# Kernel optimization log

Measured on AMD Instinct MI355X. Metric: run time of the kernel, lower is better.

Reference implementation:

```python
import jax, jax.numpy as jnp
import numpy as np

B, L = 4, 2048
D_MODEL, D_INNER, D_STATE, DT_RANK, D_CONV = 1024, 2048, 16, 64, 4


def setup_inputs() -> dict:
    key = jax.random.key(0)
    ks = jax.random.split(key, 10)
    s = lambda k, shape, sc: jax.random.normal(k, shape, dtype=jnp.float32) * sc
    return {
        "x": s(ks[0], (B, L, D_MODEL), 1.0),
        "W_in": s(ks[1], (2 * D_INNER, D_MODEL), D_MODEL ** -0.5),
        "conv_w": s(ks[2], (D_INNER, D_CONV), D_CONV ** -0.5),
        "conv_b": s(ks[3], (D_INNER,), 0.02),
        "A_log": jnp.log(jnp.arange(1, D_STATE + 1, dtype=jnp.float32)),
        "D": jnp.ones((D_INNER,), dtype=jnp.float32),
        "W_x": s(ks[4], (DT_RANK + 2 * D_STATE, D_INNER), D_INNER ** -0.5),
        "W_dt": s(ks[5], (D_INNER, DT_RANK), DT_RANK ** -0.5),
        "b_dt": s(ks[6], (D_INNER,), 0.02) - 4.0,  # softplus -> small positive dt
        "W_out": s(ks[7], (D_MODEL, D_INNER), D_INNER ** -0.5),
    }


def reference(x, W_in, conv_w, conv_b, A_log, D, W_x, W_dt, b_dt, W_out):
    Bb, Ll, _ = x.shape
    # input projection, split into ssm branch and gate branch
    xz = x @ W_in.T                       # (B, L, 2*Di)
    xr, z = jnp.split(xz, 2, axis=-1)     # (B, L, Di) each
    # depthwise causal conv1d (torch pads both sides then slices [:L])
    xc = jax.lax.conv_general_dilated(
        xr.transpose(0, 2, 1),            # (B, Di, L)
        conv_w[:, None, :],               # (Di, 1, K)
        window_strides=(1,),
        padding=[(D_CONV - 1, 0)],
        dimension_numbers=("NCH", "OIH", "NCH"),
        feature_group_count=D_INNER,
    ) + conv_b[None, :, None]
    xs = jax.nn.silu(xc.transpose(0, 2, 1))  # (B, L, Di)
    # input-dependent dt, B, C
    x_dbl = xs @ W_x.T                        # (B, L, dt_rank + 2*S)
    dt_r, b_sel, c_sel = jnp.split(x_dbl, [DT_RANK, DT_RANK + D_STATE], axis=-1)
    dt = jax.nn.softplus(dt_r @ W_dt.T + b_dt)  # (B, L, Di)
    a_diag = -jnp.exp(A_log)                    # (S,)

    def step(h, inp):
        dt_t, b_t, c_t, x_t = inp                       # (B,Di),(B,S),(B,S),(B,Di)
        a_bar = jnp.exp(dt_t[:, :, None] * a_diag)      # (B, Di, S)
        h = a_bar * h + (dt_t * x_t)[:, :, None] * b_t[:, None, :]
        y = jnp.einsum("bds,bs->bd", h, c_t) + D * x_t
        return h, y

    h0 = jnp.zeros((Bb, D_INNER, D_STATE), dtype=x.dtype)
    _, ys = jax.lax.scan(
        step, h0,
        (dt.transpose(1, 0, 2), b_sel.transpose(1, 0, 2),
         c_sel.transpose(1, 0, 2), xs.transpose(1, 0, 2)),
    )
    y = ys.transpose(1, 0, 2)                           # (B, L, Di)
    return (y * jax.nn.silu(z)) @ W_out.T               # (B, L, d_model)
```

## Files before the change

kernel.cpp:

```cpp
#include <hip/hip_runtime.h>
#include <math.h>

typedef unsigned short u16;
typedef unsigned int u32;

constexpr int Bb = 4, Ll = 2048, DM = 1024, DI = 2048, DS = 16, DTR = 64, KC = 4;
constexpr int M = Bb * Ll;
constexpr int NPAD = 128;
constexpr int NCHUNK = 32;
constexpr int LC = Ll / NCHUNK;
constexpr int LDXZ = 4096;

__device__ __forceinline__ float b2f(u16 u) {
    return __uint_as_float(((u32)u) << 16);
}
__device__ __forceinline__ u16 f2b(float f) {
    u32 x = __float_as_uint(f);
    u32 r = (x + 0x7fffu + ((x >> 16) & 1u)) >> 16;
    return (u16)r;
}
__device__ __forceinline__ float softplus_fast(float v) {
    return (v > 20.f) ? v : __logf(1.f + __expf(v));
}

typedef __attribute__((ext_vector_type(8))) short short8;
typedef __attribute__((ext_vector_type(4))) short short4v;
typedef __attribute__((ext_vector_type(4))) float floatx4;

__device__ __forceinline__ void gload16(const u16* g, u16* l) {
    __builtin_amdgcn_global_load_lds(
        (const __attribute__((address_space(1))) void*)g,
        (__attribute__((address_space(3))) void*)l,
        16, 0, 0);
}

__device__ __forceinline__ void pow_tree(float a, float* aa) {
    float a2 = a * a, a4 = a2 * a2, a8 = a4 * a4;
    aa[0] = a;        aa[1] = a2;       aa[2] = a * a2;   aa[3] = a4;
    aa[4] = a * a4;   aa[5] = a2 * a4;  aa[6] = aa[2] * a4; aa[7] = a8;
    aa[8] = a * a8;   aa[9] = a2 * a8;  aa[10] = aa[2] * a8; aa[11] = a4 * a8;
    aa[12] = aa[4] * a8; aa[13] = aa[5] * a8; aa[14] = aa[6] * a8; aa[15] = a8 * a8;
}

template<int GX, int GY>
__device__ __forceinline__ void xcd_swizzle(int& bx, int& by) {
    const int bid = blockIdx.y * GX + blockIdx.x;
    const int xcd = bid & 7;
    const int i = bid >> 3;
    const int c_local = i >> 5;
    const int within = i & 31;
    const int lx = within & 7, ly = within >> 3;
    const int chunk = xcd + c_local * 8;
    constexpr int CXN = GX / 8;
    const int cx = chunk % CXN;
    const int cy = chunk / CXN;
    bx = cx * 8 + lx;
    by = cy * 4 + ly;
}

template<int OUTM>
__global__ __launch_bounds__(512, 2) void gemm256(
    const u16* __restrict__ A, const u16* __restrict__ Bm,
    void* __restrict__ Cv,
    int K, int lda, int ldb, int ldc)
{
    __shared__ alignas(16) u16 ldsA[4][256 * 32];
    __shared__ alignas(16) u16 ldsB[4][256 * 32];

    int bx, by;
    xcd_swizzle<16, 32>(bx, by);

    const int lane = threadIdx.x & 63;
    const int wave = threadIdx.x >> 6;
    const int wr = wave >> 2;
    const int wc = wave & 3;
    const int m0 = by * 256;
    const int n0 = bx * 256;

    const int lrow = lane >> 2;
    const int skc  = (((lane & 3) + (lane >> 3)) & 3) * 8;
    const u16* pA = A  + (size_t)(m0 + wave * 32 + lrow) * lda + skc;
    const u16* pB = Bm + (size_t)(n0 + wave * 32 + lrow) * ldb + skc;
    const int ldst = wave * 1024;

    const int r16 = lane & 15;
    const int quad = lane >> 4;
    const int slot = (quad + 4 - ((r16 >> 1) & 3)) & 3;
    const int aoff = (wr * 128 + r16) * 32 + slot * 8;
    const int boff = (wc * 64  + r16) * 32 + slot * 8;

    const int NT = K >> 5;

    floatx4 acc[8][4] = {};

#pragma unroll
    for (int t = 0; t < 3; ++t) {
        gload16(pA + t * 32,            &ldsA[t][ldst]);
        gload16(pA + t * 32 + 16 * lda, &ldsA[t][ldst + 512]);
        gload16(pB + t * 32,            &ldsB[t][ldst]);
        gload16(pB + t * 32 + 16 * ldb, &ldsB[t][ldst + 512]);
    }
    asm volatile("s_waitcnt vmcnt(8)" ::: "memory");
    __builtin_amdgcn_sched_barrier(0);
    __builtin_amdgcn_s_barrier();

    for (int t = 0; t < NT; ++t) {
        const u16* la = &ldsA[t & 3][aoff];
        const u16* lb = &ldsB[t & 3][boff];
        short8 af[8], bf[4];
#pragma unroll
        for (int i = 0; i < 8; ++i) af[i] = *(const short8*)(la + i * 512);
#pragma unroll
        for (int j = 0; j < 4; ++j) bf[j] = *(const short8*)(lb + j * 512);
        if (t + 3 < NT) {
            const u16* sA = pA + (t + 3) * 32;
            const u16* sB = pB + (t + 3) * 32;
            u16* dA = &ldsA[(t + 3) & 3][ldst];
            u16* dB = &ldsB[(t + 3) & 3][ldst];
            gload16(sA, dA);
            gload16(sA + 16 * lda, dA + 512);
            gload16(sB, dB);
            gload16(sB + 16 * ldb, dB + 512);
        }
        __builtin_amdgcn_sched_barrier(0);
        __builtin_amdgcn_s_barrier();
        asm volatile("s_waitcnt lgkmcnt(0)" ::: "memory");
        __builtin_amdgcn_sched_barrier(0);
        __builtin_amdgcn_s_setprio(1);
#pragma unroll
        for (int i = 0; i < 8; ++i)
#pragma unroll
            for (int j = 0; j < 4; ++j)
                acc[i][j] = __builtin_amdgcn_mfma_f32_16x16x32_bf16(
                    af[i], bf[j], acc[i][j], 0, 0, 0);
        __builtin_amdgcn_s_setprio(0);
        if (t + 3 < NT)      asm volatile("s_waitcnt vmcnt(8)" ::: "memory");
        else if (t + 2 < NT) asm volatile("s_waitcnt vmcnt(4)" ::: "memory");
        else if (t + 1 < NT) asm volatile("s_waitcnt vmcnt(0)" ::: "memory");
        __builtin_amdgcn_sched_barrier(0);
        __builtin_amdgcn_s_barrier();
    }

    const int mw = m0 + wr * 128;
    const int nw = n0 + wc * 64;
    const int rb = quad * 4;
#pragma unroll
    for (int i = 0; i < 8; ++i) {
#pragma unroll
        for (int j = 0; j < 4; ++j) {
            const int n = nw + j * 16 + r16;
#pragma unroll
            for (int r = 0; r < 4; ++r) {
                const int m = mw + i * 16 + rb + r;
                float v = acc[i][j][r];
                if (OUTM == 1)
                    ((float*)Cv)[(size_t)m * ldc + n] = v;
                else
                    ((u16*)Cv)[(size_t)m * ldc + n] = f2b(v);
            }
        }
    }
}

template<int OUTM>
__global__ __launch_bounds__(512, 4) void gemm256n128(
    const u16* __restrict__ A, const u16* __restrict__ Bm,
    void* __restrict__ Cv,
    int K, int lda, int ldb, int ldc)
{
    __shared__ alignas(16) u16 ldsA[3][256 * 32];
    __shared__ alignas(16) u16 ldsB[3][128 * 32];

    int bx, by;
    xcd_swizzle<8, 32>(bx, by);

    const int lane = threadIdx.x & 63;
    const int wave = threadIdx.x >> 6;
    const int wr = wave >> 1;
    const int wc = wave & 1;
    const int m0 = by * 256;
    const int n0 = bx * 128;

    const int lrow = lane >> 2;
    const int skc  = (((lane & 3) + (lane >> 3)) & 3) * 8;
    const u16* pA = A  + (size_t)(m0 + wave * 32 + lrow) * lda + skc;
    const u16* pB = Bm + (size_t)(n0 + wave * 16 + lrow) * ldb + skc;
    const int ldstA = wave * 1024;
    const int ldstB = wave * 512;

    const int r16 = lane & 15;
    const int quad = lane >> 4;
    const int slot = (quad + 4 - ((r16 >> 1) & 3)) & 3;
    const int aoff = (wr * 64 + r16) * 32 + slot * 8;
    const int boff = (wc * 64 + r16) * 32 + slot * 8;

    const int NT = K >> 5;

    floatx4 acc[4][4] = {};

#pragma unroll
    for (int t = 0; t < 2; ++t) {
        gload16(pA + t * 32,            &ldsA[t][ldstA]);
        gload16(pA + t * 32 + 16 * lda, &ldsA[t][ldstA + 512]);
        gload16(pB + t * 32,            &ldsB[t][ldstB]);
    }
    asm volatile("s_waitcnt vmcnt(3)" ::: "memory");
    __builtin_amdgcn_sched_barrier(0);
    __builtin_amdgcn_s_barrier();

    int bc = 0, bs = 2;
    for (int t = 0; t < NT; ++t) {
        const u16* la = &ldsA[bc][aoff];
        const u16* lb = &ldsB[bc][boff];
        short8 af[4], bf[4];
#pragma unroll
        for (int i = 0; i < 4; ++i) af[i] = *(const short8*)(la + i * 512);
#pragma unroll
        for (int j = 0; j < 4; ++j) bf[j] = *(const short8*)(lb + j * 512);
        if (t + 2 < NT) {
            const u16* sa = pA + (t + 2) * 32;
            u16* da = &ldsA[bs][ldstA];
            gload16(sa, da);
            gload16(sa + 16 * lda, da + 512);
            gload16(pB + (t + 2) * 32, &ldsB[bs][ldstB]);
        }
        __builtin_amdgcn_sched_barrier(0);
        __builtin_amdgcn_s_barrier();
        asm volatile("s_waitcnt lgkmcnt(0)" ::: "memory");
        __builtin_amdgcn_sched_barrier(0);
        __builtin_amdgcn_s_setprio(1);
#pragma unroll
        for (int i = 0; i < 4; ++i)
#pragma unroll
            for (int j = 0; j < 4; ++j)
                acc[i][j] = __builtin_amdgcn_mfma_f32_16x16x32_bf16(
                    af[i], bf[j], acc[i][j], 0, 0, 0);
        __builtin_amdgcn_s_setprio(0);
        if (t + 2 < NT)      asm volatile("s_waitcnt vmcnt(3)" ::: "memory");
        else if (t + 1 < NT) asm volatile("s_waitcnt vmcnt(0)" ::: "memory");
        __builtin_amdgcn_sched_barrier(0);
        __builtin_amdgcn_s_barrier();
        bc = (bc == 2) ? 0 : bc + 1;
        bs = (bs == 2) ? 0 : bs + 1;
    }

    const int mw = m0 + wr * 64;
    const int nw = n0 + wc * 64;
    const int rb = quad * 4;
#pragma unroll
    for (int i = 0; i < 4; ++i) {
#pragma unroll
        for (int j = 0; j < 4; ++j) {
            const int n = nw + j * 16 + r16;
#pragma unroll
            for (int r = 0; r < 4; ++r) {
                const int m = mw + i * 16 + rb + r;
                float v = acc[i][j][r];
                if (OUTM == 1)
                    ((float*)Cv)[(size_t)m * ldc + n] = v;
                else
                    ((u16*)Cv)[(size_t)m * ldc + n] = f2b(v);
            }
        }
    }
}

template<int OUTM>
__global__ __launch_bounds__(256) void gemm_bt(
    const u16* __restrict__ A, const u16* __restrict__ Bm,
    void* __restrict__ Cv, const float* __restrict__ bias,
    int K, int lda, int ldb, int ldc)
{
    __shared__ alignas(16) u16 ldsA[128 * 32];
    __shared__ alignas(16) u16 ldsB[128 * 32];

    const int lane = threadIdx.x & 63;
    const int wave = threadIdx.x >> 6;
    const int wr = wave >> 1, wc = wave & 1;
    const int m0 = blockIdx.y * 128;
    const int n0 = blockIdx.x * 128;
    const int koff = (OUTM == 4) ? blockIdx.z * K : 0;

    const int srow = wave * 32 + (lane >> 2);
    const int skc  = (((lane & 3) + (lane >> 3)) & 3) * 8;
    const u16* Ag = A + (size_t)(m0 + srow) * lda + skc + koff;
    const u16* Bg = Bm + (size_t)(n0 + srow) * ldb + skc + koff;
    u16* lA = &ldsA[wave * 1024];
    u16* lB = &ldsB[wave * 1024];

    const int r16 = lane & 15;
    const int quad = lane >> 4;
    const int slot = (quad + 4 - ((r16 >> 1) & 3)) & 3;
    const u16* arow = &ldsA[(wr * 64 + r16) * 32 + slot * 8];
    const u16* brow = &ldsB[(wc * 64 + r16) * 32 + slot * 8];

    floatx4 acc[4][4] = {};

    for (int k0 = 0; k0 < K; k0 += 32) {
        gload16(Ag + k0,                    lA);
        gload16(Ag + k0 + (size_t)16 * lda, lA + 512);
        gload16(Bg + k0,                    lB);
        gload16(Bg + k0 + (size_t)16 * ldb, lB + 512);
        __syncthreads();

        short8 af[4], bf[4];
#pragma unroll
        for (int i = 0; i < 4; i++) af[i] = *(const short8*)(arow + i * 16 * 32);
#pragma unroll
        for (int j = 0; j < 4; j++) bf[j] = *(const short8*)(brow + j * 16 * 32);
#pragma unroll
        for (int i = 0; i < 4; i++)
#pragma unroll
            for (int j = 0; j < 4; j++)
                acc[i][j] = __builtin_amdgcn_mfma_f32_16x16x32_bf16(
                    af[i], bf[j], acc[i][j], 0, 0, 0);
        __syncthreads();
    }

    const int mw = m0 + wr * 64;
    const int nw = n0 + wc * 64;
    const int rb = quad * 4;
#pragma unroll
    for (int i = 0; i < 4; i++) {
#pragma unroll
        for (int j = 0; j < 4; j++) {
            const int n = nw + j * 16 + r16;
            if (OUTM == 4 && n >= 96) continue;
#pragma unroll
            for (int r = 0; r < 4; r++) {
                const int m = mw + i * 16 + rb + r;
                float v = acc[i][j][r];
                if (OUTM == 2)
                    v = softplus_fast(v + bias[n]);
                if (OUTM == 4)
                    ((float*)Cv)[((size_t)blockIdx.z * M + m) * ldc + n] = v;
                else if (OUTM == 1)
                    ((float*)Cv)[(size_t)m * ldc + n] = v;
                else
                    ((u16*)Cv)[(size_t)m * ldc + n] = f2b(v);
            }
        }
    }
}

__global__ __launch_bounds__(256) void redk_gemm3(
    const float* __restrict__ part, u16* __restrict__ xdbl,
    float* __restrict__ bcf)
{
    const int t = blockIdx.x * 256 + threadIdx.x;
    const int c4 = t % 24;
    const int m = t / 24;
    const int n4 = c4 * 4;
    const size_t stride = (size_t)M * NPAD;
    const float* p = part + (size_t)m * NPAD + n4;
    floatx4 acc = *(const floatx4*)(p)
                + *(const floatx4*)(p + stride)
                + *(const floatx4*)(p + 2 * stride)
                + *(const floatx4*)(p + 3 * stride);
    if (n4 < 64) {
        short4v ob;
#pragma unroll
        for (int j = 0; j < 4; j++) ob[j] = (short)f2b(acc[j]);
        *(short4v*)(xdbl + (size_t)m * 64 + n4) = ob;
    } else {
        *(floatx4*)(bcf + (size_t)m * 32 + (n4 - 64)) = acc;
    }
}

__global__ __launch_bounds__(256) void prep_all(
    const float* __restrict__ x, const float* __restrict__ W_in,
    const float* __restrict__ W_x, const float* __restrict__ W_dt,
    const float* __restrict__ W_out,
    u16* __restrict__ xbf, u16* __restrict__ wibf, u16* __restrict__ wxp,
    u16* __restrict__ wdtb, u16* __restrict__ woutb)
{
    constexpr int N0 = M * DM;
    constexpr int N1 = 2 * DI * DM;
    constexpr int N2 = NPAD * DI;
    constexpr int N3 = DI * DTR;
    int idx = blockIdx.x * blockDim.x + threadIdx.x;
    if (idx < N0) {
        xbf[idx] = f2b(x[idx]);
        return;
    }
    idx -= N0;
    if (idx < N1) {
        wibf[idx] = f2b(W_in[idx]);
    } else if (idx < N1 + N2) {
        int i = idx - N1;
        int r = i >> 11, c = i & 2047;
        wxp[i] = (r < 96) ? f2b(W_x[r * 2048 + c]) : (u16)0;
    } else if (idx < N1 + N2 + N3) {
        int i = idx - N1 - N2;
        wdtb[i] = f2b(W_dt[i]);
    } else {
        int i = idx - N1 - N2 - N3;
        woutb[i] = f2b(W_out[i]);
    }
}

__global__ __launch_bounds__(256) void conv_silu(
    const u16* __restrict__ xz, const float* __restrict__ conv_w,
    const float* __restrict__ conv_b, u16* __restrict__ xs)
{
    const int m = blockIdx.x;
    const int d0 = threadIdx.x * 8;
    const int l = m & (Ll - 1);

    float acc[8];
    {
        floatx4 cb0 = *(const floatx4*)(conv_b + d0);
        floatx4 cb1 = *(const floatx4*)(conv_b + d0 + 4);
#pragma unroll
        for (int j = 0; j < 4; j++) { acc[j] = cb0[j]; acc[4 + j] = cb1[j]; }
    }
    float w[8][KC];
#pragma unroll
    for (int jd = 0; jd < 8; jd++) {
        floatx4 wv = *(const floatx4*)(conv_w + (d0 + jd) * KC);
#pragma unroll
        for (int k = 0; k < KC; k++) w[jd][k] = wv[k];
    }
#pragma unroll
    for (int k = 0; k < KC; k++) {
        int li = l - (KC - 1) + k;
        if (li >= 0) {
            short8 xv = *(const short8*)(xz + (size_t)(m - (KC - 1) + k) * LDXZ + d0);
#pragma unroll
            for (int jd = 0; jd < 8; jd++)
                acc[jd] += b2f((u16)xv[jd]) * w[jd][k];
        }
    }
    short8 o;
#pragma unroll
    for (int jd = 0; jd < 8; jd++) {
        float s = acc[jd] / (1.f + __expf(-acc[jd]));
        o[jd] = (short)f2b(s);
    }
    *(short8*)(xs + (size_t)m * DI + d0) = o;
}

__global__ __launch_bounds__(256) void scan_p1(
    const u16* __restrict__ xzdt, const u16* __restrict__ xs,
    const float* __restrict__ bcf, const float* __restrict__ A_log,
    float* __restrict__ scr_h, float* __restrict__ sdt_g)
{
    __shared__ alignas(16) float bcs[LC * 32];

    const int d = blockIdx.x * 256 + threadIdx.x;
    const int b = blockIdx.y;
    const int c = blockIdx.z;
    const int m0 = b * Ll + c * LC;

    {
        const float* bc_g = bcf + (size_t)m0 * 32;
#pragma unroll
        for (int j = 0; j < 2; j++) {
            int idx = j * 1024 + threadIdx.x * 4;
            *(floatx4*)(bcs + idx) = *(const floatx4*)(bc_g + idx);
        }
    }

    const float ad0 = -__expf(A_log[0]);
    float adl[DS];
    bool fast = true;
#pragma unroll
    for (int s = 0; s < DS; s++) {
        float av = -__expf(A_log[s]);
        adl[s] = av;
        float kr = (float)(s + 1);
        if (fabsf(av / ad0 - kr) > 1e-4f * kr) fast = false;
    }

    const u16* dt_p = xzdt + (size_t)m0 * LDXZ + d;
    const u16* xs_p = xs + (size_t)m0 * DI + d;

    float h[DS] = {};
    float sdt = 0.f;

    __syncthreads();

    u16 dt_c = dt_p[0],     xs_c = xs_p[0];
    u16 dt_1 = dt_p[LDXZ],  xs_1 = xs_p[DI];

    if (fast) {
        for (int l = 0; l < LC; l++) {
            u16 dt_2 = dt_p[2 * LDXZ];
            u16 xs_2 = xs_p[2 * DI];
            const float* bl = bcs + l * 32;
            floatx4 B0 = *(const floatx4*)(bl);
            floatx4 B1 = *(const floatx4*)(bl + 4);
            floatx4 B2 = *(const floatx4*)(bl + 8);
            floatx4 B3 = *(const floatx4*)(bl + 12);

            float dtv = b2f(dt_c);
            float xv  = b2f(xs_c);
            float bx = dtv * xv;
            sdt += dtv;
            float aa[DS];
            pow_tree(__expf(dtv * ad0), aa);
#pragma unroll
            for (int s = 0; s < DS; s++) {
                float Bv = (s < 4) ? B0[s] : (s < 8) ? B1[s - 4]
                         : (s < 12) ? B2[s - 8] : B3[s - 12];
                h[s] = aa[s] * h[s] + bx * Bv;
            }
            dt_c = dt_1; dt_1 = dt_2; xs_c = xs_1; xs_1 = xs_2;
            dt_p += LDXZ; xs_p += DI;
        }
    } else {
        for (int l = 0; l < LC; l++) {
            u16 dt_2 = dt_p[2 * LDXZ];
            u16 xs_2 = xs_p[2 * DI];
            const float* bl = bcs + l * 32;
            floatx4 B0 = *(const floatx4*)(bl);
            floatx4 B1 = *(const floatx4*)(bl + 4);
            floatx4 B2 = *(const floatx4*)(bl + 8);
            floatx4 B3 = *(const floatx4*)(bl + 12);

            float dtv = b2f(dt_c);
            float xv  = b2f(xs_c);
            float bx = dtv * xv;
            sdt += dtv;
#pragma unroll
            for (int s = 0; s < DS; s++) {
                float Bv = (s < 4) ? B0[s] : (s < 8) ? B1[s - 4]
                         : (s < 12) ? B2[s - 8] : B3[s - 12];
                float a = __expf(dtv * adl[s]);
                h[s] = a * h[s] + bx * Bv;
            }
            dt_c = dt_1; dt_1 = dt_2; xs_c = xs_1; xs_1 = xs_2;
            dt_p += LDXZ; xs_p += DI;
        }
    }

    const size_t base = ((size_t)(b * NCHUNK + c) * DI + d) * DS;
#pragma unroll
    for (int s = 0; s < DS; s += 4) {
        floatx4 hv = {h[s], h[s+1], h[s+2], h[s+3]};
        *(floatx4*)(scr_h + base + s) = hv;
    }
    sdt_g[(size_t)(b * NCHUNK + c) * DI + d] = sdt;
}

__global__ __launch_bounds__(256) void scan_p2(
    float* __restrict__ scr_h, const float* __restrict__ sdt_g,
    const float* __restrict__ A_log)
{
    const int t = blockIdx.x * 256 + threadIdx.x;
    const int s = t & 15;
    const int d = (t >> 4) & (DI - 1);
    const int b = t >> 15;
    const float adl = -__expf(A_log[s]);

    float hin = 0.f;
    for (int c0 = 0; c0 < NCHUNK; c0 += 8) {
        float he[8], P[8];
#pragma unroll
        for (int j = 0; j < 8; j++) {
            const size_t base = ((size_t)(b * NCHUNK + c0 + j) * DI + d) * DS + s;
            he[j] = scr_h[base];
            P[j] = adl * sdt_g[(size_t)(b * NCHUNK + c0 + j) * DI + d];
        }
#pragma unroll
        for (int j = 0; j < 8; j++) P[j] = __expf(P[j]);
#pragma unroll
        for (int j = 0; j < 8; j++) {
            const size_t base = ((size_t)(b * NCHUNK + c0 + j) * DI + d) * DS + s;
            scr_h[base] = hin;
            hin = P[j] * hin + he[j];
        }
    }
}

__global__ __launch_bounds__(256) void scan_p3(
    const u16* __restrict__ xz, const u16* xs, const float* __restrict__ bcf,
    const float* __restrict__ scr_hin, const float* __restrict__ A_log,
    const float* __restrict__ Dvec, u16* yg)
{
    __shared__ alignas(16) float bcs[LC * 32];

    const int d = blockIdx.x * 256 + threadIdx.x;
    const int b = blockIdx.y;
    const int c = blockIdx.z;
    const int m0 = b * Ll + c * LC;

    {
        const float* bc_g = bcf + (size_t)m0 * 32;
#pragma unroll
        for (int j = 0; j < 2; j++) {
            int idx = j * 1024 + threadIdx.x * 4;
            *(floatx4*)(bcs + idx) = *(const floatx4*)(bc_g + idx);
        }
    }

    const float ad0 = -__expf(A_log[0]);
    float adl[DS];
    bool fast = true;
#pragma unroll
    for (int s = 0; s < DS; s++) {
        float av = -__expf(A_log[s]);
        adl[s] = av;
        float kr = (float)(s + 1);
        if (fabsf(av / ad0 - kr) > 1e-4f * kr) fast = false;
    }
    const float Dd = Dvec[d];

    const u16* dt_p = xz + (size_t)m0 * LDXZ + d;
    const u16* z_p  = xz + (size_t)m0 * LDXZ + 2048 + d;
    const u16* xs_p = xs + (size_t)m0 * DI + d;
    u16* yg_p = yg + (size_t)m0 * DI + d;

    float h[DS];
    const size_t base = ((size_t)(b * NCHUNK + c) * DI + d) * DS;
#pragma unroll
    for (int s = 0; s < DS; s += 4) {
        floatx4 hv = *(const floatx4*)(scr_hin + base + s);
        h[s] = hv[0]; h[s+1] = hv[1]; h[s+2] = hv[2]; h[s+3] = hv[3];
    }

    __syncthreads();

    u16 dt_c = dt_p[0],    dt_1 = dt_p[LDXZ];
    u16 xs_c = xs_p[0],    xs_1 = xs_p[DI];
    u16 z_c  = z_p[0],     z_1  = z_p[LDXZ];

    for (int l = 0; l < LC; l++) {
        u16 dt_2 = dt_p[2 * LDXZ];
        u16 xs_2 = xs_p[2 * DI];
        u16 z_2  = z_p[2 * LDXZ];
        const float* bl = bcs + l * 32;
        floatx4 Bq[4], Cq[4];
#pragma unroll
        for (int q = 0; q < 4; q++) {
            Bq[q] = *(const floatx4*)(bl + q * 4);
            Cq[q] = *(const floatx4*)(bl + 16 + q * 4);
        }

        float dtv = b2f(dt_c);
        float xv  = b2f(xs_c);
        float bx = dtv * xv;
        float aa[DS];
        if (fast) {
            pow_tree(__expf(dtv * ad0), aa);
        } else {
#pragma unroll
            for (int s = 0; s < DS; s++) aa[s] = __expf(dtv * adl[s]);
        }
        float y0 = 0.f, y1 = 0.f, y2 = 0.f, y3 = 0.f;
#pragma unroll
        for (int q = 0; q < 4; q++) {
#pragma unroll
            for (int j = 0; j < 4; j++) {
                int s = q * 4 + j;
                h[s] = aa[s] * h[s] + bx * Bq[q][j];
            }
        }
#pragma unroll
        for (int j = 0; j < 4; j++) {
            y0 += h[j] * Cq[0][j];
            y1 += h[4 + j] * Cq[1][j];
            y2 += h[8 + j] * Cq[2][j];
            y3 += h[12 + j] * Cq[3][j];
        }
        float yt = ((y0 + y1) + (y2 + y3)) + Dd * xv;
        float zv = b2f(z_c);
        float g = zv / (1.f + __expf(-zv));
        yg_p[0] = f2b(yt * g);

        dt_c = dt_1; dt_1 = dt_2;
        xs_c = xs_1; xs_1 = xs_2;
        z_c  = z_1;  z_1  = z_2;
        dt_p += LDXZ; xs_p += DI; z_p += LDXZ; yg_p += DI;
    }
}

extern "C" void kernel_launch(void* const* d_in, const int* in_sizes, int n_in,
                              void* d_out, int out_size, void* d_ws, size_t ws_size,
                              hipStream_t stream)
{
    const float* x      = (const float*)d_in[0];
    const float* W_in   = (const float*)d_in[1];
    const float* conv_w = (const float*)d_in[2];
    const float* conv_b = (const float*)d_in[3];
    const float* A_log  = (const float*)d_in[4];
    const float* Dvec   = (const float*)d_in[5];
    const float* W_x    = (const float*)d_in[6];
    const float* W_dt   = (const float*)d_in[7];
    const float* b_dt   = (const float*)d_in[8];
    const float* W_out  = (const float*)d_in[9];

    u16* ws = (u16*)d_ws;
    u16* xz    = ws;                 ws += (size_t)M * LDXZ;
    u16* xs    = ws;                 ws += (size_t)M * DI;
    u16* xbf   = ws;                 ws += (size_t)M * DM;
    u16* wibf  = ws;                 ws += (size_t)2 * DI * DM;
    u16* wxp   = ws;                 ws += (size_t)NPAD * DI;
    u16* wdtb  = ws;                 ws += (size_t)DI * DTR;
    u16* woutb = ws;                 ws += (size_t)DM * DI;
    u16* xdbl  = ws;                 ws += (size_t)M * NPAD;
    float* part  = (float*)xbf;
    float* scr_h = (float*)xbf;
    float* bcf   = (float*)wibf;
    float* sdt_g = bcf + (size_t)M * 32;

    {
        constexpr int NTOT = M * DM + 2 * DI * DM + NPAD * DI + DI * DTR + DM * DI;
        prep_all<<<NTOT / 256, 256, 0, stream>>>(
            x, W_in, W_x, W_dt, W_out, xbf, wibf, wxp, wdtb, woutb);
    }

    gemm256<0><<<dim3(LDXZ / 256, M / 256), 512, 0, stream>>>(
        xbf, wibf, xz, DM, DM, DM, LDXZ);

    conv_silu<<<M, 256, 0, stream>>>(xz, conv_w, conv_b, xs);

    gemm_bt<4><<<dim3(1, M / 128, 4), 256, 0, stream>>>(
        xs, wxp, part, nullptr, DI / 4, DI, DI, NPAD);
    redk_gemm3<<<(M * 24) / 256, 256, 0, stream>>>(part, xdbl, bcf);

    gemm_bt<2><<<dim3(DI / 128, M / 128), 256, 0, stream>>>(
        xdbl, wdtb, xz, b_dt, DTR, 64, DTR, LDXZ);

    scan_p1<<<dim3(DI / 256, Bb, NCHUNK), 256, 0, stream>>>(
        xz, xs, bcf, A_log, scr_h, sdt_g);
    scan_p2<<<(Bb * DI * DS) / 256, 256, 0, stream>>>(scr_h, sdt_g, A_log);
    scan_p3<<<dim3(DI / 256, Bb, NCHUNK), 256, 0, stream>>>(
        xz, xs, bcf, scr_h, A_log, Dvec, xs);

    gemm256n128<1><<<dim3(DM / 128, M / 256), 512, 0, stream>>>(
        xs, woutb, d_out, DI, DI, DI, DM);
}
```

Measured before the change: 415.5 us.

## Deepen out-projection GEMM pipeline and tile conv over 8 timesteps

The out-projection GEMM now processes two K-tiles per barrier pair with a six-deep LDS ring and four tiles in flight. This halves the number of barriers and deepens global-load prefetch, at the cost of doubled LDS (about 144KB) and lower occupancy, with launch bounds reduced to 2 blocks. Separately, the causal conv+SiLU kernel now handles 8 consecutive timesteps per block with a sliding window of 11 loaded rows instead of 4 loads per output row, which cuts redundant global reads of xz.

```diff
diff --git a/kernel.cpp b/kernel.cpp
--- a/kernel.cpp
+++ b/kernel.cpp
@@ -163,13 +163,13 @@
 }
 
 template<int OUTM>
-__global__ __launch_bounds__(512, 4) void gemm256n128(
+__global__ __launch_bounds__(512, 2) void gemm256n128(
     const u16* __restrict__ A, const u16* __restrict__ Bm,
     void* __restrict__ Cv,
     int K, int lda, int ldb, int ldc)
 {
-    __shared__ alignas(16) u16 ldsA[3][256 * 32];
-    __shared__ alignas(16) u16 ldsB[3][128 * 32];
+    __shared__ alignas(16) u16 ldsA[6][256 * 32];
+    __shared__ alignas(16) u16 ldsB[6][128 * 32];
 
     int bx, by;
     xcd_swizzle<8, 32>(bx, by);
@@ -195,34 +195,46 @@
     const int boff = (wc * 64 + r16) * 32 + slot * 8;
 
     const int NT = K >> 5;
+    const int NP = NT >> 1;
 
     floatx4 acc[4][4] = {};
 
 #pragma unroll
-    for (int t = 0; t < 2; ++t) {
+    for (int t = 0; t < 4; ++t) {
         gload16(pA + t * 32,            &ldsA[t][ldstA]);
         gload16(pA + t * 32 + 16 * lda, &ldsA[t][ldstA + 512]);
         gload16(pB + t * 32,            &ldsB[t][ldstB]);
     }
-    asm volatile("s_waitcnt vmcnt(3)" ::: "memory");
+    asm volatile("s_waitcnt vmcnt(6)" ::: "memory");
     __builtin_amdgcn_sched_barrier(0);
     __builtin_amdgcn_s_barrier();
 
-    int bc = 0, bs = 2;
-    for (int t = 0; t < NT; ++t) {
-        const u16* la = &ldsA[bc][aoff];
-        const u16* lb = &ldsB[bc][boff];
-        short8 af[4], bf[4];
-#pragma unroll
-        for (int i = 0; i < 4; ++i) af[i] = *(const short8*)(la + i * 512);
-#pragma unroll
-        for (int j = 0; j < 4; ++j) bf[j] = *(const short8*)(lb + j * 512);
-        if (t + 2 < NT) {
-            const u16* sa = pA + (t + 2) * 32;
-            u16* da = &ldsA[bs][ldstA];
-            gload16(sa, da);
-            gload16(sa + 16 * lda, da + 512);
-            gload16(pB + (t + 2) * 32, &ldsB[bs][ldstB]);
+    int b0 = 0, b1 = 1, s0 = 4, s1 = 5;
+    for (int p = 0; p < NP; ++p) {
+        const int t0 = 2 * p;
+        const u16* la0 = &ldsA[b0][aoff];
+        const u16* lb0 = &ldsB[b0][boff];
+        const u16* la1 = &ldsA[b1][aoff];
+        const u16* lb1 = &ldsB[b1][boff];
+        short8 af0[4], bf0[4], af1[4], bf1[4];
+#pragma unroll
+        for (int i = 0; i < 4; ++i) {
+            af0[i] = *(const short8*)(la0 + i * 512);
+            af1[i] = *(const short8*)(la1 + i * 512);
+            bf0[i] = *(const short8*)(lb0 + i * 512);
+            bf1[i] = *(const short8*)(lb1 + i * 512);
+        }
+        if (t0 + 4 < NT) {
+            const u16* sa0 = pA + (t0 + 4) * 32;
+            const u16* sa1 = pA + (t0 + 5) * 32;
+            u16* da0 = &ldsA[s0][ldstA];
+            u16* da1 = &ldsA[s1][ldstA];
+            gload16(sa0, da0);
+            gload16(sa0 + 16 * lda, da0 + 512);
+            gload16(pB + (t0 + 4) * 32, &ldsB[s0][ldstB]);
+            gload16(sa1, da1);
+            gload16(sa1 + 16 * lda, da1 + 512);
+            gload16(pB + (t0 + 5) * 32, &ldsB[s1][ldstB]);
         }
         __builtin_amdgcn_sched_barrier(0);
         __builtin_amdgcn_s_barrier();
@@ -234,14 +246,22 @@
 #pragma unroll
             for (int j = 0; j < 4; ++j)
                 acc[i][j] = __builtin_amdgcn_mfma_f32_16x16x32_bf16(
-                    af[i], bf[j], acc[i][j], 0, 0, 0);
+                    af0[i], bf0[j], acc[i][j], 0, 0, 0);
+#pragma unroll
+        for (int i = 0; i < 4; ++i)
+#pragma unroll
+            for (int j = 0; j < 4; ++j)
+                acc[i][j] = __builtin_amdgcn_mfma_f32_16x16x32_bf16(
+                    af1[i], bf1[j], acc[i][j], 0, 0, 0);
         __builtin_amdgcn_s_setprio(0);
-        if (t + 2 < NT)      asm volatile("s_waitcnt vmcnt(3)" ::: "memory");
-        else if (t + 1 < NT) asm volatile("s_waitcnt vmcnt(0)" ::: "memory");
+        if (t0 + 4 < NT)      asm volatile("s_waitcnt vmcnt(6)" ::: "memory");
+        else if (t0 + 2 < NT) asm volatile("s_waitcnt vmcnt(0)" ::: "memory");
         __builtin_amdgcn_sched_barrier(0);
         __builtin_amdgcn_s_barrier();
-        bc = (bc == 2) ? 0 : bc + 1;
-        bs = (bs == 2) ? 0 : bs + 1;
+        b0 += 2; if (b0 >= 6) b0 -= 6;
+        b1 += 2; if (b1 >= 6) b1 -= 6;
+        s0 += 2; if (s0 >= 6) s0 -= 6;
+        s1 += 2; if (s1 >= 6) s1 -= 6;
     }
 
     const int mw = m0 + wr * 64;
@@ -399,45 +419,59 @@
     }
 }
 
-__global__ __launch_bounds__(256) void conv_silu(
+__global__ __launch_bounds__(256) void conv_silu8(
     const u16* __restrict__ xz, const float* __restrict__ conv_w,
     const float* __restrict__ conv_b, u16* __restrict__ xs)
 {
-    const int m = blockIdx.x;
+    const int m0 = blockIdx.x * 8;
     const int d0 = threadIdx.x * 8;
-    const int l = m & (Ll - 1);
-
-    float acc[8];
+    const int l0 = m0 & (Ll - 1);
+
+    short8 xv[11];
+#pragma unroll
+    for (int j = 0; j < 11; j++) {
+        if (l0 + j >= 3) {
+            xv[j] = *(const short8*)(xz + (size_t)(m0 - 3 + j) * LDXZ + d0);
+        } else {
+#pragma unroll
+            for (int e = 0; e < 8; e++) xv[j][e] = 0;
+        }
+    }
+
+    float w[8][KC];
+#pragma unroll
+    for (int jd = 0; jd < 8; jd++) {
+        floatx4 wv = *(const floatx4*)(conv_w + (d0 + jd) * KC);
+#pragma unroll
+        for (int k = 0; k < KC; k++) w[jd][k] = wv[k];
+    }
+    float cb[8];
     {
         floatx4 cb0 = *(const floatx4*)(conv_b + d0);
         floatx4 cb1 = *(const floatx4*)(conv_b + d0 + 4);
 #pragma unroll
-        for (int j = 0; j < 4; j++) { acc[j] = cb0[j]; acc[4 + j] = cb1[j]; }
-    }
-    float w[8][KC];
-#pragma unroll
-    for (int jd = 0; jd < 8; jd++) {
-        floatx4 wv = *(const floatx4*)(conv_w + (d0 + jd) * KC);
-#pragma unroll
-        for (int k = 0; k < KC; k++) w[jd][k] = wv[k];
-    }
-#pragma unroll
-    for (int k = 0; k < KC; k++) {
-        int li = l - (KC - 1) + k;
-        if (li >= 0) {
-            short8 xv = *(const short8*)(xz + (size_t)(m - (KC - 1) + k) * LDXZ + d0);
+        for (int j = 0; j < 4; j++) { cb[j] = cb0[j]; cb[4 + j] = cb1[j]; }
+    }
+
+#pragma unroll
+    for (int j = 0; j < 8; j++) {
+        float acc[8];
+#pragma unroll
+        for (int jd = 0; jd < 8; jd++) acc[jd] = cb[jd];
+#pragma unroll
+        for (int k = 0; k < KC; k++) {
 #pragma unroll
             for (int jd = 0; jd < 8; jd++)
-                acc[jd] += b2f((u16)xv[jd]) * w[jd][k];
-        }
-    }
-    short8 o;
-#pragma unroll
-    for (int jd = 0; jd < 8; jd++) {
-        float s = acc[jd] / (1.f + __expf(-acc[jd]));
-        o[jd] = (short)f2b(s);
-    }
-    *(short8*)(xs + (size_t)m * DI + d0) = o;
+                acc[jd] += b2f((u16)xv[j + k][jd]) * w[jd][k];
+        }
+        short8 o;
+#pragma unroll
+        for (int jd = 0; jd < 8; jd++) {
+            float s = acc[jd] / (1.f + __expf(-acc[jd]));
+            o[jd] = (short)f2b(s);
+        }
+        *(short8*)(xs + (size_t)(m0 + j) * DI + d0) = o;
+    }
 }
 
 __global__ __launch_bounds__(256) void scan_p1(
@@ -713,7 +747,7 @@
     gemm256<0><<<dim3(LDXZ / 256, M / 256), 512, 0, stream>>>(
         xbf, wibf, xz, DM, DM, DM, LDXZ);
 
-    conv_silu<<<M, 256, 0, stream>>>(xz, conv_w, conv_b, xs);
+    conv_silu8<<<M / 8, 256, 0, stream>>>(xz, conv_w, conv_b, xs);
 
     gemm_bt<4><<<dim3(1, M / 128, 4), 256, 0, stream>>>(
         xs, wxp, part, nullptr, DI / 4, DI, DI, NPAD);
```

Result: faster. 394.5 us (-5.0%).
